# Kernel tuning notes

Measured on AMD Instinct MI355X. Metric: run time of the kernel, lower is better.

Reference implementation:

```python
import jax, jax.numpy as jnp
import numpy as np

N, D_IN, D_OUT, E, K, H = 8192, 256, 256, 16, 2, 512


def setup_inputs() -> dict:
    key = jax.random.key(0)
    ks = jax.random.split(key, 11)
    return {
        "x": jax.random.normal(ks[0], (N, D_IN), jnp.float32),
        "gate_w": jax.random.normal(ks[1], (D_IN, H), jnp.float32),
        "gate_b": jax.random.normal(ks[2], (H,), jnp.float32),
        "gate_out_w": jax.random.normal(ks[3], (H, E), jnp.float32),
        "gate_out_b": jax.random.normal(ks[4], (E,), jnp.float32),
        "mlp_w1": jax.random.normal(ks[5], (D_IN, E, H), jnp.float32),
        "mlp_b1": jax.random.normal(ks[6], (E, H), jnp.float32),
        "mlp_w2": jax.random.normal(ks[7], (H, E, H), jnp.float32),
        "mlp_b2": jax.random.normal(ks[8], (E, H), jnp.float32),
        "mlp_w3": jax.random.normal(ks[9], (H, E, D_OUT), jnp.float32),
        "mlp_b3": jax.random.normal(ks[10], (E, D_OUT), jnp.float32),
    }


def reference(x, gate_w, gate_b, gate_out_w, gate_out_b,
              mlp_w1, mlp_b1, mlp_w2, mlp_b2, mlp_w3, mlp_b3):
    n, e = x.shape[0], gate_out_w.shape[1]
    # Gate MLP: relu(x @ Wg + bg) @ Wo + bo -> [N, E]
    logits = jax.nn.relu(x @ gate_w + gate_b) @ gate_out_w + gate_out_b
    # Top-k expert selection + softmax over selected gate values
    top_vals, top_idx = jax.lax.top_k(logits, K)              # [N, K]
    gates = jax.nn.softmax(top_vals, axis=-1)                 # [N, K]
    # Scatter into a sparse combine matrix [N, E] (top-k indices are unique per row)
    combine = jnp.zeros((n, e), x.dtype).at[jnp.arange(n)[:, None], top_idx].set(gates)
    # Per-expert 3-layer MLP, computed densely over all experts then combined.
    h1 = jax.nn.relu(jnp.einsum('ni,ieh->neh', x, mlp_w1) + mlp_b1)    # [N, E, H]
    h2 = jax.nn.relu(jnp.einsum('neh,heg->neg', h1, mlp_w2) + mlp_b2)  # [N, E, H]
    ye = jnp.einsum('neg,geo->neo', h2, mlp_w3) + mlp_b3               # [N, E, D_OUT]
    # Gate-weighted combine over experts (only top-k contribute)
    return jnp.einsum('neo,ne->no', ye, combine)
```

## Files before the change

kernel.cpp:

```cpp
#include <hip/hip_runtime.h>
#include <hip/hip_bf16.h>
#include <stdint.h>

#define NTOK 8192
#define DIN  256
#define DOUT 256
#define NEXP 16
#define HID  512
#define NKA  (NTOK*2)
#define NBLK (NTOK/256)
#define MAXTILE 272
#define GK 768

typedef __bf16 bf16x8 __attribute__((ext_vector_type(8)));
typedef __bf16 bf16x4 __attribute__((ext_vector_type(4)));
typedef float  f32x4  __attribute__((ext_vector_type(4)));

__device__ __forceinline__ void async_cp16(const __bf16* g, __bf16* l) {
  __builtin_amdgcn_global_load_lds(
      (const __attribute__((address_space(1))) unsigned int*)g,
      (__attribute__((address_space(3))) unsigned int*)l, 16, 0, 0);
}

__global__ void cvt_x_kernel(const float* __restrict__ x, __bf16* __restrict__ xb,
                             __bf16* __restrict__ xs) {
  int i = blockIdx.x * blockDim.x + threadIdx.x;
  float4 v = ((const float4*)x)[i];
  int base = i * 4;
  int t = base >> 8, c = base & 255;
  bf16x4 hi = { (__bf16)v.x, (__bf16)v.y, (__bf16)v.z, (__bf16)v.w };
  bf16x4 lo = { (__bf16)(v.x - (float)hi[0]), (__bf16)(v.y - (float)hi[1]),
                (__bf16)(v.z - (float)hi[2]), (__bf16)(v.w - (float)hi[3]) };
  *(bf16x4*)(xb + (size_t)t * DIN + c) = hi;
  __bf16* row = xs + (size_t)t * GK + c;
  *(bf16x4*)(row)       = hi;
  *(bf16x4*)(row + 256) = lo;
  *(bf16x4*)(row + 512) = hi;
}

__global__ void transpose_cvt_kernel(const float* __restrict__ src, __bf16* __restrict__ dst,
                                     int K, int N) {
  __shared__ float t[32][33];
  int e  = blockIdx.z;
  int k0 = blockIdx.x * 32, n0 = blockIdx.y * 32;
  int tx = threadIdx.x, ty = threadIdx.y;
  #pragma unroll
  for (int j = 0; j < 4; j++) {
    int kl = ty + j * 8;
    t[kl][tx] = src[(size_t)(k0 + kl) * (NEXP * N) + (size_t)e * N + n0 + tx];
  }
  __syncthreads();
  #pragma unroll
  for (int j = 0; j < 4; j++) {
    int nl = ty + j * 8;
    dst[(size_t)e * N * K + (size_t)(n0 + nl) * K + k0 + tx] = (__bf16)t[tx][nl];
  }
}

__global__ void gate_w_split_kernel(const float* __restrict__ gw, __bf16* __restrict__ gwt,
                                    int* __restrict__ gtile_e, int* __restrict__ gtile_mt,
                                    int* __restrict__ gntiles, int* __restrict__ gseg) {
  __shared__ float t[32][33];
  int k0 = blockIdx.x * 32, n0 = blockIdx.y * 32;
  int tx = threadIdx.x, ty = threadIdx.y;
  #pragma unroll
  for (int j = 0; j < 4; j++) {
    int kl = ty + j * 8;
    t[kl][tx] = gw[(size_t)(k0 + kl) * HID + n0 + tx];
  }
  __syncthreads();
  #pragma unroll
  for (int j = 0; j < 4; j++) {
    int nl = ty + j * 8;
    float v = t[tx][nl];
    __bf16 hi = (__bf16)v;
    __bf16 lo = (__bf16)(v - (float)hi);
    __bf16* drow = gwt + (size_t)(n0 + nl) * GK + k0 + tx;
    drow[0]   = hi;
    drow[256] = hi;
    drow[512] = lo;
  }
  if (blockIdx.x == 0 && blockIdx.y == 0) {
    int tid = ty * 32 + tx;
    if (tid < 128) { gtile_e[tid] = 0; gtile_mt[tid] = tid; }
    else if (tid == 128) { *gntiles = 128; }
    else if (tid == 129) { gseg[0] = 0; gseg[1] = NTOK; }
  }
}

__global__ __launch_bounds__(128) void logits_kernel(const float* __restrict__ hg,
                                                     const float* __restrict__ gw,
                                                     const float* __restrict__ gb,
                                                     float* __restrict__ logits) {
  __shared__ float hl[8][HID];
  __shared__ float wl[HID][16];
  int t0 = blockIdx.x * 8;
  int tid = threadIdx.x;
  for (int c = tid; c < 8 * (HID / 4); c += 128) {
    int row = c >> 7, col = (c & 127) * 4;
    *(float4*)&hl[row][col] = *(const float4*)&hg[(size_t)(t0 + row) * HID + col];
  }
  for (int c = tid; c < HID * 4; c += 128) {
    int k = c >> 2, e4 = (c & 3) * 4;
    *(float4*)&wl[k][e4] = *(const float4*)&gw[(size_t)k * 16 + e4];
  }
  __syncthreads();
  int tok = tid >> 4, e = tid & 15;
  float s = gb[e];
  #pragma unroll 8
  for (int k = 0; k < HID; k++) s = fmaf(hl[tok][k], wl[k][e], s);
  logits[(size_t)(t0 + tok) * 16 + e] = s;
}

__global__ __launch_bounds__(256) void top2_route_kernel(const float* __restrict__ logits,
                                                         int2* __restrict__ e01,
                                                         float2* __restrict__ g01,
                                                         int* __restrict__ lrank,
                                                         int* __restrict__ blockhist) {
  __shared__ int hist[NEXP];
  int tid = threadIdx.x;
  if (tid < NEXP) hist[tid] = 0;
  __syncthreads();
  int t = blockIdx.x * 256 + tid;
  float lv[16];
  const float4* lp = (const float4*)(logits + (size_t)t * 16);
  #pragma unroll
  for (int j = 0; j < 4; j++) { float4 v = lp[j]; lv[4*j]=v.x; lv[4*j+1]=v.y; lv[4*j+2]=v.z; lv[4*j+3]=v.w; }
  float v0 = -3.402823466e38f, v1 = -3.402823466e38f;
  int i0 = 0, i1 = 0;
  #pragma unroll
  for (int e = 0; e < 16; e++) {
    float v = lv[e];
    if (v > v0) { v1 = v0; i1 = i0; v0 = v; i0 = e; }
    else if (v > v1) { v1 = v; i1 = e; }
  }
  float ew = expf(v1 - v0);
  float inv = 1.f / (1.f + ew);
  e01[t] = make_int2(i0, i1);
  g01[t] = make_float2(inv, ew * inv);
  int r0 = atomicAdd(&hist[i0], 1);
  int r1 = atomicAdd(&hist[i1], 1);
  lrank[2 * t]     = r0;
  lrank[2 * t + 1] = r1;
  __syncthreads();
  if (tid < NEXP) blockhist[blockIdx.x * NEXP + tid] = hist[tid];
}

__global__ void scan2_kernel(const int* __restrict__ blockhist, int* __restrict__ offsets,
                             int* __restrict__ base, int* __restrict__ tile_e,
                             int* __restrict__ tile_mt, int* __restrict__ ntiles) {
  __shared__ int tot[NEXP];
  __shared__ int soff[NEXP + 1];
  __shared__ int tbase[NEXP];
  int e = threadIdx.x;
  if (e < NEXP) {
    int s = 0;
    for (int b = 0; b < NBLK; b++) s += blockhist[b * NEXP + e];
    tot[e] = s;
  }
  __syncthreads();
  if (e == 0) {
    int s = 0, tb = 0;
    for (int i = 0; i < NEXP; i++) {
      soff[i] = s; s += tot[i];
      tbase[i] = tb; tb += (tot[i] + 63) >> 6;
    }
    soff[NEXP] = s;
    *ntiles = tb;
  }
  __syncthreads();
  if (e < NEXP + 1) offsets[e] = soff[e];
  if (e < NEXP) {
    int s = soff[e];
    for (int b = 0; b < NBLK; b++) { base[b * NEXP + e] = s; s += blockhist[b * NEXP + e]; }
    int nt = (tot[e] + 63) >> 6, tb = tbase[e];
    for (int m = 0; m < nt; m++) { tile_e[tb + m] = e; tile_mt[tb + m] = m; }
  }
}

__global__ __launch_bounds__(256) void fill2_kernel(const int2* __restrict__ e01,
                                                    const int* __restrict__ lrank,
                                                    const int* __restrict__ base,
                                                    int* __restrict__ tok_sorted,
                                                    int* __restrict__ route_pos) {
  int b = blockIdx.x;
  int t = b * 256 + threadIdx.x;
  int2 e = e01[t];
  int p0 = base[b * NEXP + e.x] + lrank[2 * t];
  int p1 = base[b * NEXP + e.y] + lrank[2 * t + 1];
  tok_sorted[p0] = t; route_pos[2 * t]     = p0;
  tok_sorted[p1] = t; route_pos[2 * t + 1] = p1;
}

template<bool OUT_F32, bool RELU>
__global__ __launch_bounds__(256) void moe_gemm_kernel(const __bf16* __restrict__ A,
                                                       const __bf16* __restrict__ Bt,
                                                       const float* __restrict__ bias,
                                                       void* __restrict__ out,
                                                       const int* __restrict__ seg_off,
                                                       const int* __restrict__ gather,
                                                       const int* __restrict__ tile_e,
                                                       const int* __restrict__ tile_mt,
                                                       const int* __restrict__ ntiles,
                                                       int K, int N) {
  int bx = blockIdx.x;
  if (bx >= *ntiles) return;
  int e  = tile_e[bx];
  int mt = tile_mt[bx];
  int off = seg_off[e];
  int Te  = seg_off[e + 1] - off;
  int nt = blockIdx.y;

  __shared__ __bf16 Al[2][64][32];
  __shared__ __bf16 Bl[2][128][32];

  int tid = threadIdx.x;
  int lane = tid & 63, w = tid >> 6;
  int l16 = lane & 15, quad = lane >> 4;

  int r0 = tid >> 2;
  int q8 = ((tid & 3) ^ ((r0 >> 1) & 3)) * 8;
  int rowA = mt * 64 + r0;
  int rA = rowA < Te ? rowA : Te - 1;
  size_t ga = gather ? (size_t)gather[off + rA] : (size_t)(off + rA);
  const __bf16* apg  = A + ga * K + q8;
  const __bf16* Bte  = Bt + (size_t)e * N * K;
  const __bf16* bpg0 = Bte + (size_t)(nt * 128 + r0) * K + q8;
  const __bf16* bpg1 = bpg0 + (size_t)64 * K;

  __bf16* al0 = &Al[0][0][0];
  __bf16* al1 = &Al[1][0][0];
  __bf16* bl0 = &Bl[0][0][0];
  __bf16* bl1 = &Bl[1][0][0];

  f32x4 acc[4][2];
  #pragma unroll
  for (int i = 0; i < 4; i++)
    #pragma unroll
    for (int j = 0; j < 2; j++) acc[i][j] = {0.f, 0.f, 0.f, 0.f};

  async_cp16(apg, al0 + tid * 8);
  async_cp16(bpg0, bl0 + tid * 8);
  async_cp16(bpg1, bl0 + (tid + 256) * 8);

  int qs = (quad ^ ((l16 >> 1) & 3)) * 8;

  int nIter = K >> 5;
  for (int it = 0; it < nIter; ++it) {
    int buf = it & 1;
    if (it + 1 < nIter) {
      int kb = (it + 1) << 5;
      __bf16* an = buf ? al0 : al1;
      __bf16* bn = buf ? bl0 : bl1;
      async_cp16(apg + kb, an + tid * 8);
      async_cp16(bpg0 + kb, bn + tid * 8);
      async_cp16(bpg1 + kb, bn + (tid + 256) * 8);
      asm volatile("s_waitcnt vmcnt(3)" ::: "memory");
    } else {
      asm volatile("s_waitcnt vmcnt(0)" ::: "memory");
    }
    __builtin_amdgcn_s_barrier();
    asm volatile("" ::: "memory");
    const __bf16* ab = buf ? al1 : al0;
    const __bf16* bb = buf ? bl1 : bl0;
    bf16x8 af[4], bfr[2];
    #pragma unroll
    for (int i = 0; i < 4; i++)
      af[i] = *(const bf16x8*)(ab + (size_t)(i * 16 + l16) * 32 + qs);
    #pragma unroll
    for (int i = 0; i < 2; i++)
      bfr[i] = *(const bf16x8*)(bb + (size_t)(w * 32 + i * 16 + l16) * 32 + qs);
    #pragma unroll
    for (int mi = 0; mi < 4; mi++)
      #pragma unroll
      for (int ni = 0; ni < 2; ni++)
        acc[mi][ni] = __builtin_amdgcn_mfma_f32_16x16x32_bf16(af[mi], bfr[ni], acc[mi][ni], 0, 0, 0);
    asm volatile("" ::: "memory");
    __builtin_amdgcn_s_barrier();
  }

  const float* be = bias + (size_t)e * N;
  #pragma unroll
  for (int ni = 0; ni < 2; ni++) {
    int col = nt * 128 + w * 32 + ni * 16 + l16;
    float bv = be[col];
    #pragma unroll
    for (int mi = 0; mi < 4; mi++) {
      #pragma unroll
      for (int r = 0; r < 4; r++) {
        int row_in = mt * 64 + mi * 16 + quad * 4 + r;
        if (row_in < Te) {
          float v = acc[mi][ni][r] + bv;
          if (RELU) v = fmaxf(v, 0.f);
          size_t orow = (size_t)(off + row_in);
          if (OUT_F32) ((float*)out)[orow * N + col] = v;
          else ((__bf16*)out)[orow * N + col] = (__bf16)v;
        }
      }
    }
  }
}

__global__ void combine_kernel(const float* __restrict__ Y, const int* __restrict__ route_pos,
                               const float2* __restrict__ g01, float* __restrict__ out) {
  int gid = blockIdx.x * blockDim.x + threadIdx.x;
  int t = gid >> 6, c = (gid & 63) << 2;
  if (t >= NTOK) return;
  int p0 = route_pos[2 * t], p1 = route_pos[2 * t + 1];
  float2 g = g01[t];
  float4 y0 = *(const float4*)&Y[(size_t)p0 * DOUT + c];
  float4 y1 = *(const float4*)&Y[(size_t)p1 * DOUT + c];
  float4 o;
  o.x = g.x * y0.x + g.y * y1.x;
  o.y = g.x * y0.y + g.y * y1.y;
  o.z = g.x * y0.z + g.y * y1.z;
  o.w = g.x * y0.w + g.y * y1.w;
  *(float4*)&out[(size_t)t * DOUT + c] = o;
}

extern "C" void kernel_launch(void* const* d_in, const int* in_sizes, int n_in,
                              void* d_out, int out_size, void* d_ws, size_t ws_size,
                              hipStream_t stream) {
  const float* x          = (const float*)d_in[0];
  const float* gate_w     = (const float*)d_in[1];
  const float* gate_b     = (const float*)d_in[2];
  const float* gate_out_w = (const float*)d_in[3];
  const float* gate_out_b = (const float*)d_in[4];
  const float* w1         = (const float*)d_in[5];
  const float* b1         = (const float*)d_in[6];
  const float* w2         = (const float*)d_in[7];
  const float* b2         = (const float*)d_in[8];
  const float* w3         = (const float*)d_in[9];
  const float* b3         = (const float*)d_in[10];
  float* out = (float*)d_out;

  char* ws = (char*)d_ws;
  size_t o = 0;
  auto alloc = [&](size_t bytes) -> void* {
    o = (o + 255) & ~(size_t)255;
    void* p = ws + o;
    o += bytes;
    return p;
  };

  __bf16* xb   = (__bf16*)alloc((size_t)NTOK * DIN * 2);
  __bf16* w1t  = (__bf16*)alloc((size_t)NEXP * HID * DIN * 2);
  __bf16* w2t  = (__bf16*)alloc((size_t)NEXP * HID * HID * 2);
  __bf16* w3t  = (__bf16*)alloc((size_t)NEXP * DOUT * HID * 2);
  __bf16* gwt  = (__bf16*)alloc((size_t)HID * GK * 2);
  size_t r1 = (size_t)NTOK * HID * 4;
  size_t r2 = (size_t)(NKA + 128) * HID * 2;
  void* region1 = alloc(r1 > r2 ? r1 : r2);
  float*  hg = (float*)region1;
  __bf16* H1 = (__bf16*)region1;
  size_t r3 = (size_t)NTOK * GK * 2;
  size_t r4 = (size_t)(NKA + 128) * HID * 2;
  void* region2 = alloc(r3 > r4 ? r3 : r4);
  __bf16* xs = (__bf16*)region2;
  __bf16* H2 = (__bf16*)region2;
  float* logits    = (float*)alloc((size_t)NTOK * 16 * 4);
  int2*  e01       = (int2*)alloc((size_t)NTOK * 8);
  float2* g01      = (float2*)alloc((size_t)NTOK * 8);
  int*   offsets   = (int*)alloc((NEXP + 1) * 4);
  int*   blockhist = (int*)alloc((size_t)NBLK * NEXP * 4);
  int*   base      = (int*)alloc((size_t)NBLK * NEXP * 4);
  int*   lrank     = (int*)alloc((size_t)NTOK * 2 * 4);
  int*   tok_sorted= (int*)alloc((size_t)(NKA + 128) * 4);
  int*   route_pos = (int*)alloc((size_t)NTOK * 2 * 4);
  int*   tile_e    = (int*)alloc(MAXTILE * 4);
  int*   tile_mt   = (int*)alloc(MAXTILE * 4);
  int*   ntiles    = (int*)alloc(4);
  int*   gtile_e   = (int*)alloc(128 * 4);
  int*   gtile_mt  = (int*)alloc(128 * 4);
  int*   gntiles   = (int*)alloc(4);
  int*   gseg      = (int*)alloc(2 * 4);
  float*  Y        = (float*)alloc((size_t)(NKA + 128) * DOUT * 4);
  (void)ws_size; (void)n_in; (void)in_sizes; (void)out_size;

  cvt_x_kernel<<<(NTOK * DIN / 4) / 256, 256, 0, stream>>>(x, xb, xs);

  dim3 tb(32, 8);
  gate_w_split_kernel<<<dim3(DIN / 32, HID / 32), tb, 0, stream>>>(
      gate_w, gwt, gtile_e, gtile_mt, gntiles, gseg);
  transpose_cvt_kernel<<<dim3(DIN / 32, HID / 32, NEXP), tb, 0, stream>>>(w1, w1t, DIN, HID);
  transpose_cvt_kernel<<<dim3(HID / 32, HID / 32, NEXP), tb, 0, stream>>>(w2, w2t, HID, HID);
  transpose_cvt_kernel<<<dim3(HID / 32, DOUT / 32, NEXP), tb, 0, stream>>>(w3, w3t, HID, DOUT);

  moe_gemm_kernel<true, true><<<dim3(NTOK / 64, HID / 128), 256, 0, stream>>>(
      xs, gwt, gate_b, hg, gseg, nullptr, gtile_e, gtile_mt, gntiles, GK, HID);

  logits_kernel<<<NTOK / 8, 128, 0, stream>>>(hg, gate_out_w, gate_out_b, logits);
  top2_route_kernel<<<NBLK, 256, 0, stream>>>(logits, e01, g01, lrank, blockhist);
  scan2_kernel<<<1, 64, 0, stream>>>(blockhist, offsets, base, tile_e, tile_mt, ntiles);
  fill2_kernel<<<NBLK, 256, 0, stream>>>(e01, lrank, base, tok_sorted, route_pos);

  moe_gemm_kernel<false, true><<<dim3(MAXTILE, HID / 128), 256, 0, stream>>>(
      xb, w1t, b1, H1, offsets, tok_sorted, tile_e, tile_mt, ntiles, DIN, HID);
  moe_gemm_kernel<false, true><<<dim3(MAXTILE, HID / 128), 256, 0, stream>>>(
      H1, w2t, b2, H2, offsets, nullptr, tile_e, tile_mt, ntiles, HID, HID);
  moe_gemm_kernel<true, false><<<dim3(MAXTILE, DOUT / 128), 256, 0, stream>>>(
      H2, w3t, b3, Y, offsets, nullptr, tile_e, tile_mt, ntiles, HID, DOUT);

  combine_kernel<<<(NTOK * 64) / 256, 256, 0, stream>>>(Y, route_pos, g01, out);
}
```

Measured before the change: 233.1 us.

## Fuse prep conversions into one launch and merge logits with top-2 routing

All input and weight conversion kernels (x split, gate weight split, three expert weight transposes) are merged into a single prep_kernel dispatched by block index. This cuts four launches and their gaps. The logits and top-2 routing kernels are fused into a route_kernel that keeps logits in shared memory, removing the logits buffer round trip. Histograms are now per 8-token block (1024 blocks), so the scan kernel is parallelised over 256 threads with a two-level prefix, and fill2 indexes base by t>>3.

After: 223.8 us. -4.0%, faster.

```diff
diff --git a/kernel.cpp b/kernel.cpp
--- a/kernel.cpp
+++ b/kernel.cpp
@@ -9,6 +9,7 @@
 #define HID  512
 #define NKA  (NTOK*2)
 #define NBLK (NTOK/256)
+#define NRBLK (NTOK/8)
 #define MAXTILE 272
 #define GK 768
 
@@ -22,28 +23,11 @@
       (__attribute__((address_space(3))) unsigned int*)l, 16, 0, 0);
 }
 
-__global__ void cvt_x_kernel(const float* __restrict__ x, __bf16* __restrict__ xb,
-                             __bf16* __restrict__ xs) {
-  int i = blockIdx.x * blockDim.x + threadIdx.x;
-  float4 v = ((const float4*)x)[i];
-  int base = i * 4;
-  int t = base >> 8, c = base & 255;
-  bf16x4 hi = { (__bf16)v.x, (__bf16)v.y, (__bf16)v.z, (__bf16)v.w };
-  bf16x4 lo = { (__bf16)(v.x - (float)hi[0]), (__bf16)(v.y - (float)hi[1]),
-                (__bf16)(v.z - (float)hi[2]), (__bf16)(v.w - (float)hi[3]) };
-  *(bf16x4*)(xb + (size_t)t * DIN + c) = hi;
-  __bf16* row = xs + (size_t)t * GK + c;
-  *(bf16x4*)(row)       = hi;
-  *(bf16x4*)(row + 256) = lo;
-  *(bf16x4*)(row + 512) = hi;
-}
-
-__global__ void transpose_cvt_kernel(const float* __restrict__ src, __bf16* __restrict__ dst,
-                                     int K, int N) {
-  __shared__ float t[32][33];
-  int e  = blockIdx.z;
-  int k0 = blockIdx.x * 32, n0 = blockIdx.y * 32;
-  int tx = threadIdx.x, ty = threadIdx.y;
+__device__ __forceinline__ void transpose_cvt_body(const float* __restrict__ src,
+                                                   __bf16* __restrict__ dst,
+                                                   int K, int N, int bx, int by, int bz,
+                                                   int tx, int ty, float (*t)[33]) {
+  int e = bz, k0 = bx * 32, n0 = by * 32;
   #pragma unroll
   for (int j = 0; j < 4; j++) {
     int kl = ty + j * 8;
@@ -57,45 +41,82 @@
   }
 }
 
-__global__ void gate_w_split_kernel(const float* __restrict__ gw, __bf16* __restrict__ gwt,
-                                    int* __restrict__ gtile_e, int* __restrict__ gtile_mt,
-                                    int* __restrict__ gntiles, int* __restrict__ gseg) {
+__global__ __launch_bounds__(256) void prep_kernel(
+    const float* __restrict__ x, __bf16* __restrict__ xb, __bf16* __restrict__ xs,
+    const float* __restrict__ gw, __bf16* __restrict__ gwt,
+    const float* __restrict__ w1, __bf16* __restrict__ w1t,
+    const float* __restrict__ w2, __bf16* __restrict__ w2t,
+    const float* __restrict__ w3, __bf16* __restrict__ w3t,
+    int* __restrict__ gtile_e, int* __restrict__ gtile_mt,
+    int* __restrict__ gntiles, int* __restrict__ gseg) {
   __shared__ float t[32][33];
-  int k0 = blockIdx.x * 32, n0 = blockIdx.y * 32;
-  int tx = threadIdx.x, ty = threadIdx.y;
-  #pragma unroll
-  for (int j = 0; j < 4; j++) {
-    int kl = ty + j * 8;
-    t[kl][tx] = gw[(size_t)(k0 + kl) * HID + n0 + tx];
-  }
-  __syncthreads();
-  #pragma unroll
-  for (int j = 0; j < 4; j++) {
-    int nl = ty + j * 8;
-    float v = t[tx][nl];
-    __bf16 hi = (__bf16)v;
-    __bf16 lo = (__bf16)(v - (float)hi);
-    __bf16* drow = gwt + (size_t)(n0 + nl) * GK + k0 + tx;
-    drow[0]   = hi;
-    drow[256] = hi;
-    drow[512] = lo;
-  }
-  if (blockIdx.x == 0 && blockIdx.y == 0) {
-    int tid = ty * 32 + tx;
-    if (tid < 128) { gtile_e[tid] = 0; gtile_mt[tid] = tid; }
-    else if (tid == 128) { *gntiles = 128; }
-    else if (tid == 129) { gseg[0] = 0; gseg[1] = NTOK; }
-  }
-}
-
-__global__ __launch_bounds__(128) void logits_kernel(const float* __restrict__ hg,
-                                                     const float* __restrict__ gw,
-                                                     const float* __restrict__ gb,
-                                                     float* __restrict__ logits) {
-  __shared__ float hl[8][HID];
+  int idx = blockIdx.x;
+  int tid = threadIdx.x;
+  int tx = tid & 31, ty = tid >> 5;
+  if (idx < 2048) {
+    int i = idx * 256 + tid;
+    float4 v = ((const float4*)x)[i];
+    int base = i * 4;
+    int tk = base >> 8, c = base & 255;
+    bf16x4 hi = { (__bf16)v.x, (__bf16)v.y, (__bf16)v.z, (__bf16)v.w };
+    bf16x4 lo = { (__bf16)(v.x - (float)hi[0]), (__bf16)(v.y - (float)hi[1]),
+                  (__bf16)(v.z - (float)hi[2]), (__bf16)(v.w - (float)hi[3]) };
+    *(bf16x4*)(xb + (size_t)tk * DIN + c) = hi;
+    __bf16* row = xs + (size_t)tk * GK + c;
+    *(bf16x4*)(row)       = hi;
+    *(bf16x4*)(row + 256) = lo;
+    *(bf16x4*)(row + 512) = hi;
+  } else if (idx < 2176) {
+    int g = idx - 2048;
+    int k0 = (g & 7) * 32, n0 = (g >> 3) * 32;
+    #pragma unroll
+    for (int j = 0; j < 4; j++) {
+      int kl = ty + j * 8;
+      t[kl][tx] = gw[(size_t)(k0 + kl) * HID + n0 + tx];
+    }
+    __syncthreads();
+    #pragma unroll
+    for (int j = 0; j < 4; j++) {
+      int nl = ty + j * 8;
+      float v = t[tx][nl];
+      __bf16 hi = (__bf16)v;
+      __bf16 lo = (__bf16)(v - (float)hi);
+      __bf16* drow = gwt + (size_t)(n0 + nl) * GK + k0 + tx;
+      drow[0]   = hi;
+      drow[256] = hi;
+      drow[512] = lo;
+    }
+    if (g == 0) {
+      if (tid < 128) { gtile_e[tid] = 0; gtile_mt[tid] = tid; }
+      else if (tid == 128) { *gntiles = 128; }
+      else if (tid == 129) { gseg[0] = 0; gseg[1] = NTOK; }
+    }
+  } else if (idx < 4224) {
+    int g = idx - 2176;
+    transpose_cvt_body(w1, w1t, DIN, HID, g & 7, (g >> 3) & 15, g >> 7, tx, ty, t);
+  } else if (idx < 8320) {
+    int g = idx - 4224;
+    transpose_cvt_body(w2, w2t, HID, HID, g & 15, (g >> 4) & 15, g >> 8, tx, ty, t);
+  } else {
+    int g = idx - 8320;
+    transpose_cvt_body(w3, w3t, HID, DOUT, g & 15, (g >> 4) & 7, g >> 7, tx, ty, t);
+  }
+}
+
+__global__ __launch_bounds__(128) void route_kernel(const float* __restrict__ hg,
+                                                    const float* __restrict__ gw,
+                                                    const float* __restrict__ gb,
+                                                    int2* __restrict__ e01,
+                                                    float2* __restrict__ g01,
+                                                    int* __restrict__ lrank,
+                                                    int* __restrict__ blockhist) {
+  __shared__ float hl[8][HID + 8];
   __shared__ float wl[HID][16];
+  __shared__ float ls[8][16];
+  __shared__ int bhist[NEXP];
   int t0 = blockIdx.x * 8;
   int tid = threadIdx.x;
+  if (tid < NEXP) bhist[tid] = 0;
   for (int c = tid; c < 8 * (HID / 4); c += 128) {
     int row = c >> 7, col = (c & 127) * 4;
     *(float4*)&hl[row][col] = *(const float4*)&hg[(size_t)(t0 + row) * HID + col];
@@ -109,72 +130,76 @@
   float s = gb[e];
   #pragma unroll 8
   for (int k = 0; k < HID; k++) s = fmaf(hl[tok][k], wl[k][e], s);
-  logits[(size_t)(t0 + tok) * 16 + e] = s;
-}
-
-__global__ __launch_bounds__(256) void top2_route_kernel(const float* __restrict__ logits,
-                                                         int2* __restrict__ e01,
-                                                         float2* __restrict__ g01,
-                                                         int* __restrict__ lrank,
-                                                         int* __restrict__ blockhist) {
-  __shared__ int hist[NEXP];
-  int tid = threadIdx.x;
-  if (tid < NEXP) hist[tid] = 0;
-  __syncthreads();
-  int t = blockIdx.x * 256 + tid;
-  float lv[16];
-  const float4* lp = (const float4*)(logits + (size_t)t * 16);
-  #pragma unroll
-  for (int j = 0; j < 4; j++) { float4 v = lp[j]; lv[4*j]=v.x; lv[4*j+1]=v.y; lv[4*j+2]=v.z; lv[4*j+3]=v.w; }
-  float v0 = -3.402823466e38f, v1 = -3.402823466e38f;
-  int i0 = 0, i1 = 0;
-  #pragma unroll
-  for (int e = 0; e < 16; e++) {
-    float v = lv[e];
-    if (v > v0) { v1 = v0; i1 = i0; v0 = v; i0 = e; }
-    else if (v > v1) { v1 = v; i1 = e; }
-  }
-  float ew = expf(v1 - v0);
-  float inv = 1.f / (1.f + ew);
-  e01[t] = make_int2(i0, i1);
-  g01[t] = make_float2(inv, ew * inv);
-  int r0 = atomicAdd(&hist[i0], 1);
-  int r1 = atomicAdd(&hist[i1], 1);
-  lrank[2 * t]     = r0;
-  lrank[2 * t + 1] = r1;
-  __syncthreads();
-  if (tid < NEXP) blockhist[blockIdx.x * NEXP + tid] = hist[tid];
-}
-
-__global__ void scan2_kernel(const int* __restrict__ blockhist, int* __restrict__ offsets,
-                             int* __restrict__ base, int* __restrict__ tile_e,
-                             int* __restrict__ tile_mt, int* __restrict__ ntiles) {
+  ls[tok][e] = s;
+  __syncthreads();
+  if (tid < 8) {
+    int t = t0 + tid;
+    float v0 = -3.402823466e38f, v1 = -3.402823466e38f;
+    int i0 = 0, i1 = 0;
+    #pragma unroll
+    for (int ee = 0; ee < 16; ee++) {
+      float v = ls[tid][ee];
+      if (v > v0) { v1 = v0; i1 = i0; v0 = v; i0 = ee; }
+      else if (v > v1) { v1 = v; i1 = ee; }
+    }
+    float ew = expf(v1 - v0);
+    float inv = 1.f / (1.f + ew);
+    e01[t] = make_int2(i0, i1);
+    g01[t] = make_float2(inv, ew * inv);
+    int r0 = atomicAdd(&bhist[i0], 1);
+    int r1 = atomicAdd(&bhist[i1], 1);
+    lrank[2 * t]     = r0;
+    lrank[2 * t + 1] = r1;
+  }
+  __syncthreads();
+  if (tid < NEXP) blockhist[blockIdx.x * NEXP + tid] = bhist[tid];
+}
+
+__global__ __launch_bounds__(256) void scan2_kernel(const int* __restrict__ blockhist,
+                                                    int* __restrict__ offsets,
+                                                    int* __restrict__ base,
+                                                    int* __restrict__ tile_e,
+                                                    int* __restrict__ tile_mt,
+                                                    int* __restrict__ ntiles) {
+  __shared__ int part[NEXP][16];
+  __shared__ int cbase[NEXP][16];
   __shared__ int tot[NEXP];
   __shared__ int soff[NEXP + 1];
   __shared__ int tbase[NEXP];
-  int e = threadIdx.x;
-  if (e < NEXP) {
-    int s = 0;
-    for (int b = 0; b < NBLK; b++) s += blockhist[b * NEXP + e];
-    tot[e] = s;
-  }
-  __syncthreads();
-  if (e == 0) {
-    int s = 0, tb = 0;
+  int tid = threadIdx.x;
+  int e = tid & 15, c = tid >> 4;
+  int s = 0;
+  for (int i = 0; i < 64; i++) s += blockhist[(size_t)(c * 64 + i) * NEXP + e];
+  part[e][c] = s;
+  __syncthreads();
+  if (tid < NEXP) {
+    int t = 0;
+    for (int c2 = 0; c2 < 16; c2++) { cbase[tid][c2] = t; t += part[tid][c2]; }
+    tot[tid] = t;
+  }
+  __syncthreads();
+  if (tid == 0) {
+    int acc = 0, tb = 0;
     for (int i = 0; i < NEXP; i++) {
-      soff[i] = s; s += tot[i];
+      soff[i] = acc; acc += tot[i];
       tbase[i] = tb; tb += (tot[i] + 63) >> 6;
     }
-    soff[NEXP] = s;
+    soff[NEXP] = acc;
     *ntiles = tb;
   }
   __syncthreads();
-  if (e < NEXP + 1) offsets[e] = soff[e];
-  if (e < NEXP) {
-    int s = soff[e];
-    for (int b = 0; b < NBLK; b++) { base[b * NEXP + e] = s; s += blockhist[b * NEXP + e]; }
-    int nt = (tot[e] + 63) >> 6, tb = tbase[e];
-    for (int m = 0; m < nt; m++) { tile_e[tb + m] = e; tile_mt[tb + m] = m; }
+  if (tid < NEXP + 1) offsets[tid] = soff[tid];
+  {
+    int run = soff[e] + cbase[e][c];
+    for (int i = 0; i < 64; i++) {
+      int b = c * 64 + i;
+      base[(size_t)b * NEXP + e] = run;
+      run += blockhist[(size_t)b * NEXP + e];
+    }
+  }
+  if (tid < NEXP) {
+    int nt = (tot[tid] + 63) >> 6, tb = tbase[tid];
+    for (int m = 0; m < nt; m++) { tile_e[tb + m] = tid; tile_mt[tb + m] = m; }
   }
 }
 
@@ -183,11 +208,11 @@
                                                     const int* __restrict__ base,
                                                     int* __restrict__ tok_sorted,
                                                     int* __restrict__ route_pos) {
-  int b = blockIdx.x;
-  int t = b * 256 + threadIdx.x;
+  int t = blockIdx.x * 256 + threadIdx.x;
   int2 e = e01[t];
-  int p0 = base[b * NEXP + e.x] + lrank[2 * t];
-  int p1 = base[b * NEXP + e.y] + lrank[2 * t + 1];
+  int b = t >> 3;
+  int p0 = base[(size_t)b * NEXP + e.x] + lrank[2 * t];
+  int p1 = base[(size_t)b * NEXP + e.y] + lrank[2 * t + 1];
   tok_sorted[p0] = t; route_pos[2 * t]     = p0;
   tok_sorted[p1] = t; route_pos[2 * t + 1] = p1;
 }
@@ -358,12 +383,11 @@
   void* region2 = alloc(r3 > r4 ? r3 : r4);
   __bf16* xs = (__bf16*)region2;
   __bf16* H2 = (__bf16*)region2;
-  float* logits    = (float*)alloc((size_t)NTOK * 16 * 4);
   int2*  e01       = (int2*)alloc((size_t)NTOK * 8);
   float2* g01      = (float2*)alloc((size_t)NTOK * 8);
   int*   offsets   = (int*)alloc((NEXP + 1) * 4);
-  int*   blockhist = (int*)alloc((size_t)NBLK * NEXP * 4);
-  int*   base      = (int*)alloc((size_t)NBLK * NEXP * 4);
+  int*   blockhist = (int*)alloc((size_t)NRBLK * NEXP * 4);
+  int*   base      = (int*)alloc((size_t)NRBLK * NEXP * 4);
   int*   lrank     = (int*)alloc((size_t)NTOK * 2 * 4);
   int*   tok_sorted= (int*)alloc((size_t)(NKA + 128) * 4);
   int*   route_pos = (int*)alloc((size_t)NTOK * 2 * 4);
@@ -377,21 +401,16 @@
   float*  Y        = (float*)alloc((size_t)(NKA + 128) * DOUT * 4);
   (void)ws_size; (void)n_in; (void)in_sizes; (void)out_size;
 
-  cvt_x_kernel<<<(NTOK * DIN / 4) / 256, 256, 0, stream>>>(x, xb, xs);
-
-  dim3 tb(32, 8);
-  gate_w_split_kernel<<<dim3(DIN / 32, HID / 32), tb, 0, stream>>>(
-      gate_w, gwt, gtile_e, gtile_mt, gntiles, gseg);
-  transpose_cvt_kernel<<<dim3(DIN / 32, HID / 32, NEXP), tb, 0, stream>>>(w1, w1t, DIN, HID);
-  transpose_cvt_kernel<<<dim3(HID / 32, HID / 32, NEXP), tb, 0, stream>>>(w2, w2t, HID, HID);
-  transpose_cvt_kernel<<<dim3(HID / 32, DOUT / 32, NEXP), tb, 0, stream>>>(w3, w3t, HID, DOUT);
+  prep_kernel<<<10368, 256, 0, stream>>>(x, xb, xs, gate_w, gwt,
+                                         w1, w1t, w2, w2t, w3, w3t,
+                                         gtile_e, gtile_mt, gntiles, gseg);
 
   moe_gemm_kernel<true, true><<<dim3(NTOK / 64, HID / 128), 256, 0, stream>>>(
       xs, gwt, gate_b, hg, gseg, nullptr, gtile_e, gtile_mt, gntiles, GK, HID);
 
-  logits_kernel<<<NTOK / 8, 128, 0, stream>>>(hg, gate_out_w, gate_out_b, logits);
-  top2_route_kernel<<<NBLK, 256, 0, stream>>>(logits, e01, g01, lrank, blockhist);
-  scan2_kernel<<<1, 64, 0, stream>>>(blockhist, offsets, base, tile_e, tile_mt, ntiles);
+  route_kernel<<<NTOK / 8, 128, 0, stream>>>(hg, gate_out_w, gate_out_b,
+                                             e01, g01, lrank, blockhist);
+  scan2_kernel<<<1, 256, 0, stream>>>(blockhist, offsets, base, tile_e, tile_mt, ntiles);
   fill2_kernel<<<NBLK, 256, 0, stream>>>(e01, lrank, base, tok_sorted, route_pos);
 
   moe_gemm_kernel<false, true><<<dim3(MAXTILE, HID / 128), 256, 0, stream>>>(
```

## Merge prep kernels into one launch and fuse gate logits into gate GEMM epilogue

Applied to the files above, without the earlier changes.

Folds the x conversion, gate-weight split, three expert-weight transposes and a logits zero-fill into a single prep kernel keyed on block index. This cuts several launches and their tail gaps. The gate GEMM now does the second gate layer in its epilogue: the ReLU hidden tile goes to LDS, is multiplied by a slice of gate_out_w, and partial logits are atomically added. That removes the fp32 hidden-state write/read and the separate logits kernel, with the output bias moved into top2. The cost is float atomics, which make logit sums order-nondeterministic and could in rare cases flip top-2 ties.

Result: faster. 202.5 us (-13.1%).

```diff
diff --git a/kernel.cpp b/kernel.cpp
--- a/kernel.cpp
+++ b/kernel.cpp
@@ -22,28 +22,11 @@
       (__attribute__((address_space(3))) unsigned int*)l, 16, 0, 0);
 }
 
-__global__ void cvt_x_kernel(const float* __restrict__ x, __bf16* __restrict__ xb,
-                             __bf16* __restrict__ xs) {
-  int i = blockIdx.x * blockDim.x + threadIdx.x;
-  float4 v = ((const float4*)x)[i];
-  int base = i * 4;
-  int t = base >> 8, c = base & 255;
-  bf16x4 hi = { (__bf16)v.x, (__bf16)v.y, (__bf16)v.z, (__bf16)v.w };
-  bf16x4 lo = { (__bf16)(v.x - (float)hi[0]), (__bf16)(v.y - (float)hi[1]),
-                (__bf16)(v.z - (float)hi[2]), (__bf16)(v.w - (float)hi[3]) };
-  *(bf16x4*)(xb + (size_t)t * DIN + c) = hi;
-  __bf16* row = xs + (size_t)t * GK + c;
-  *(bf16x4*)(row)       = hi;
-  *(bf16x4*)(row + 256) = lo;
-  *(bf16x4*)(row + 512) = hi;
-}
-
-__global__ void transpose_cvt_kernel(const float* __restrict__ src, __bf16* __restrict__ dst,
-                                     int K, int N) {
-  __shared__ float t[32][33];
-  int e  = blockIdx.z;
-  int k0 = blockIdx.x * 32, n0 = blockIdx.y * 32;
-  int tx = threadIdx.x, ty = threadIdx.y;
+__device__ __forceinline__ void transpose_cvt_body(const float* __restrict__ src,
+                                                   __bf16* __restrict__ dst,
+                                                   int K, int N, int bx, int by, int bz,
+                                                   int tx, int ty, float (*t)[33]) {
+  int e = bz, k0 = bx * 32, n0 = by * 32;
   #pragma unroll
   for (int j = 0; j < 4; j++) {
     int kl = ty + j * 8;
@@ -57,75 +40,94 @@
   }
 }
 
-__global__ void gate_w_split_kernel(const float* __restrict__ gw, __bf16* __restrict__ gwt,
-                                    int* __restrict__ gtile_e, int* __restrict__ gtile_mt,
-                                    int* __restrict__ gntiles, int* __restrict__ gseg) {
+__global__ __launch_bounds__(256) void prep_kernel(
+    const float* __restrict__ x, __bf16* __restrict__ xb, __bf16* __restrict__ xs,
+    const float* __restrict__ gw, __bf16* __restrict__ gwt,
+    const float* __restrict__ w1, __bf16* __restrict__ w1t,
+    const float* __restrict__ w2, __bf16* __restrict__ w2t,
+    const float* __restrict__ w3, __bf16* __restrict__ w3t,
+    int* __restrict__ gtile_e, int* __restrict__ gtile_mt,
+    int* __restrict__ gntiles, int* __restrict__ gseg,
+    float* __restrict__ logitz) {
   __shared__ float t[32][33];
-  int k0 = blockIdx.x * 32, n0 = blockIdx.y * 32;
-  int tx = threadIdx.x, ty = threadIdx.y;
-  #pragma unroll
-  for (int j = 0; j < 4; j++) {
-    int kl = ty + j * 8;
-    t[kl][tx] = gw[(size_t)(k0 + kl) * HID + n0 + tx];
-  }
-  __syncthreads();
-  #pragma unroll
-  for (int j = 0; j < 4; j++) {
-    int nl = ty + j * 8;
-    float v = t[tx][nl];
-    __bf16 hi = (__bf16)v;
-    __bf16 lo = (__bf16)(v - (float)hi);
-    __bf16* drow = gwt + (size_t)(n0 + nl) * GK + k0 + tx;
-    drow[0]   = hi;
-    drow[256] = hi;
-    drow[512] = lo;
-  }
-  if (blockIdx.x == 0 && blockIdx.y == 0) {
-    int tid = ty * 32 + tx;
-    if (tid < 128) { gtile_e[tid] = 0; gtile_mt[tid] = tid; }
-    else if (tid == 128) { *gntiles = 128; }
-    else if (tid == 129) { gseg[0] = 0; gseg[1] = NTOK; }
-  }
-}
-
-__global__ __launch_bounds__(128) void logits_kernel(const float* __restrict__ hg,
-                                                     const float* __restrict__ gw,
-                                                     const float* __restrict__ gb,
-                                                     float* __restrict__ logits) {
-  __shared__ float hl[8][HID];
-  __shared__ float wl[HID][16];
-  int t0 = blockIdx.x * 8;
+  int idx = blockIdx.x;
   int tid = threadIdx.x;
-  for (int c = tid; c < 8 * (HID / 4); c += 128) {
-    int row = c >> 7, col = (c & 127) * 4;
-    *(float4*)&hl[row][col] = *(const float4*)&hg[(size_t)(t0 + row) * HID + col];
-  }
-  for (int c = tid; c < HID * 4; c += 128) {
-    int k = c >> 2, e4 = (c & 3) * 4;
-    *(float4*)&wl[k][e4] = *(const float4*)&gw[(size_t)k * 16 + e4];
-  }
-  __syncthreads();
-  int tok = tid >> 4, e = tid & 15;
-  float s = gb[e];
-  #pragma unroll 8
-  for (int k = 0; k < HID; k++) s = fmaf(hl[tok][k], wl[k][e], s);
-  logits[(size_t)(t0 + tok) * 16 + e] = s;
-}
-
-__global__ __launch_bounds__(256) void top2_route_kernel(const float* __restrict__ logits,
-                                                         int2* __restrict__ e01,
-                                                         float2* __restrict__ g01,
-                                                         int* __restrict__ lrank,
-                                                         int* __restrict__ blockhist) {
+  int tx = tid & 31, ty = tid >> 5;
+  if (idx < 2048) {
+    int i = idx * 256 + tid;
+    float4 v = ((const float4*)x)[i];
+    int base = i * 4;
+    int tk = base >> 8, c = base & 255;
+    bf16x4 hi = { (__bf16)v.x, (__bf16)v.y, (__bf16)v.z, (__bf16)v.w };
+    bf16x4 lo = { (__bf16)(v.x - (float)hi[0]), (__bf16)(v.y - (float)hi[1]),
+                  (__bf16)(v.z - (float)hi[2]), (__bf16)(v.w - (float)hi[3]) };
+    *(bf16x4*)(xb + (size_t)tk * DIN + c) = hi;
+    __bf16* row = xs + (size_t)tk * GK + c;
+    *(bf16x4*)(row)       = hi;
+    *(bf16x4*)(row + 256) = lo;
+    *(bf16x4*)(row + 512) = hi;
+  } else if (idx < 2176) {
+    int g = idx - 2048;
+    int k0 = (g & 7) * 32, n0 = (g >> 3) * 32;
+    #pragma unroll
+    for (int j = 0; j < 4; j++) {
+      int kl = ty + j * 8;
+      t[kl][tx] = gw[(size_t)(k0 + kl) * HID + n0 + tx];
+    }
+    __syncthreads();
+    #pragma unroll
+    for (int j = 0; j < 4; j++) {
+      int nl = ty + j * 8;
+      float v = t[tx][nl];
+      __bf16 hi = (__bf16)v;
+      __bf16 lo = (__bf16)(v - (float)hi);
+      __bf16* drow = gwt + (size_t)(n0 + nl) * GK + k0 + tx;
+      drow[0]   = hi;
+      drow[256] = hi;
+      drow[512] = lo;
+    }
+    if (g == 0) {
+      if (tid < 128) { gtile_e[tid] = 0; gtile_mt[tid] = tid; }
+      else if (tid == 128) { *gntiles = 128; }
+      else if (tid == 129) { gseg[0] = 0; gseg[1] = NTOK; }
+    }
+  } else if (idx < 4224) {
+    int g = idx - 2176;
+    transpose_cvt_body(w1, w1t, DIN, HID, g & 7, (g >> 3) & 15, g >> 7, tx, ty, t);
+  } else if (idx < 8320) {
+    int g = idx - 4224;
+    transpose_cvt_body(w2, w2t, HID, HID, g & 15, (g >> 4) & 15, g >> 8, tx, ty, t);
+  } else if (idx < 10368) {
+    int g = idx - 8320;
+    transpose_cvt_body(w3, w3t, HID, DOUT, g & 15, (g >> 4) & 7, g >> 7, tx, ty, t);
+  } else {
+    int i = (idx - 10368) * 256 + tid;
+    ((float4*)logitz)[i] = make_float4(0.f, 0.f, 0.f, 0.f);
+  }
+}
+
+__global__ __launch_bounds__(256) void top2_kernel(const float* __restrict__ logits,
+                                                   const float* __restrict__ gb,
+                                                   int2* __restrict__ e01,
+                                                   float2* __restrict__ g01,
+                                                   int* __restrict__ lrank,
+                                                   int* __restrict__ blockhist) {
   __shared__ int hist[NEXP];
+  __shared__ float gbl[NEXP];
   int tid = threadIdx.x;
-  if (tid < NEXP) hist[tid] = 0;
+  if (tid < NEXP) { hist[tid] = 0; gbl[tid] = gb[tid]; }
   __syncthreads();
   int t = blockIdx.x * 256 + tid;
   float lv[16];
   const float4* lp = (const float4*)(logits + (size_t)t * 16);
   #pragma unroll
-  for (int j = 0; j < 4; j++) { float4 v = lp[j]; lv[4*j]=v.x; lv[4*j+1]=v.y; lv[4*j+2]=v.z; lv[4*j+3]=v.w; }
+  for (int j = 0; j < 4; j++) {
+    float4 v = lp[j];
+    lv[4*j]   = v.x + gbl[4*j];
+    lv[4*j+1] = v.y + gbl[4*j+1];
+    lv[4*j+2] = v.z + gbl[4*j+2];
+    lv[4*j+3] = v.w + gbl[4*j+3];
+  }
   float v0 = -3.402823466e38f, v1 = -3.402823466e38f;
   int i0 = 0, i1 = 0;
   #pragma unroll
@@ -192,7 +194,7 @@
   tok_sorted[p1] = t; route_pos[2 * t + 1] = p1;
 }
 
-template<bool OUT_F32, bool RELU>
+template<int MODE, bool RELU>
 __global__ __launch_bounds__(256) void moe_gemm_kernel(const __bf16* __restrict__ A,
                                                        const __bf16* __restrict__ Bt,
                                                        const float* __restrict__ bias,
@@ -202,6 +204,7 @@
                                                        const int* __restrict__ tile_e,
                                                        const int* __restrict__ tile_mt,
                                                        const int* __restrict__ ntiles,
+                                                       const float* __restrict__ gow,
                                                        int K, int N) {
   int bx = blockIdx.x;
   if (bx >= *ntiles) return;
@@ -211,8 +214,10 @@
   int Te  = seg_off[e + 1] - off;
   int nt = blockIdx.y;
 
-  __shared__ __bf16 Al[2][64][32];
-  __shared__ __bf16 Bl[2][128][32];
+  constexpr int SMEM = (MODE == 3) ? (8192 + 64 * 132 * 4) : 24576;
+  __shared__ __align__(16) char smem[SMEM];
+  __bf16* AlB = (__bf16*)smem;
+  __bf16* BlB = (__bf16*)(smem + 8192);
 
   int tid = threadIdx.x;
   int lane = tid & 63, w = tid >> 6;
@@ -228,10 +233,10 @@
   const __bf16* bpg0 = Bte + (size_t)(nt * 128 + r0) * K + q8;
   const __bf16* bpg1 = bpg0 + (size_t)64 * K;
 
-  __bf16* al0 = &Al[0][0][0];
-  __bf16* al1 = &Al[1][0][0];
-  __bf16* bl0 = &Bl[0][0][0];
-  __bf16* bl1 = &Bl[1][0][0];
+  __bf16* al0 = AlB;
+  __bf16* al1 = AlB + 2048;
+  __bf16* bl0 = BlB;
+  __bf16* bl1 = BlB + 4096;
 
   f32x4 acc[4][2];
   #pragma unroll
@@ -280,6 +285,49 @@
   }
 
   const float* be = bias + (size_t)e * N;
+  if (MODE == 3) {
+    __syncthreads();
+    float* wl = (float*)smem;
+    float* ht = (float*)(smem + 8192);
+    if (tid < 128) {
+      const float* gr = gow + (size_t)(nt * 128 + tid) * 16;
+      #pragma unroll
+      for (int j = 0; j < 4; j++)
+        *(float4*)&wl[tid * 16 + j * 4] = *(const float4*)&gr[j * 4];
+    }
+    float bv[2];
+    #pragma unroll
+    for (int ni = 0; ni < 2; ni++) bv[ni] = be[nt * 128 + w * 32 + ni * 16 + l16];
+    #pragma unroll
+    for (int mi = 0; mi < 4; mi++)
+      #pragma unroll
+      for (int ni = 0; ni < 2; ni++)
+        #pragma unroll
+        for (int r = 0; r < 4; r++) {
+          int row = mi * 16 + quad * 4 + r;
+          int col = w * 32 + ni * 16 + l16;
+          ht[row * 132 + col] = fmaxf(acc[mi][ni][r] + bv[ni], 0.f);
+        }
+    __syncthreads();
+    int t = tid >> 2, e4 = (tid & 3) * 4;
+    float s0 = 0.f, s1 = 0.f, s2 = 0.f, s3 = 0.f;
+    #pragma unroll 4
+    for (int h = 0; h < 128; h++) {
+      float hv = ht[t * 132 + h];
+      const float* wr = &wl[h * 16 + e4];
+      s0 = fmaf(hv, wr[0], s0);
+      s1 = fmaf(hv, wr[1], s1);
+      s2 = fmaf(hv, wr[2], s2);
+      s3 = fmaf(hv, wr[3], s3);
+    }
+    float* lp = (float*)out + (size_t)(mt * 64 + t) * 16 + e4;
+    atomicAdd(lp + 0, s0);
+    atomicAdd(lp + 1, s1);
+    atomicAdd(lp + 2, s2);
+    atomicAdd(lp + 3, s3);
+    return;
+  }
+
   #pragma unroll
   for (int ni = 0; ni < 2; ni++) {
     int col = nt * 128 + w * 32 + ni * 16 + l16;
@@ -293,7 +341,7 @@
           float v = acc[mi][ni][r] + bv;
           if (RELU) v = fmaxf(v, 0.f);
           size_t orow = (size_t)(off + row_in);
-          if (OUT_F32) ((float*)out)[orow * N + col] = v;
+          if (MODE == 1) ((float*)out)[orow * N + col] = v;
           else ((__bf16*)out)[orow * N + col] = (__bf16)v;
         }
       }
@@ -348,11 +396,7 @@
   __bf16* w2t  = (__bf16*)alloc((size_t)NEXP * HID * HID * 2);
   __bf16* w3t  = (__bf16*)alloc((size_t)NEXP * DOUT * HID * 2);
   __bf16* gwt  = (__bf16*)alloc((size_t)HID * GK * 2);
-  size_t r1 = (size_t)NTOK * HID * 4;
-  size_t r2 = (size_t)(NKA + 128) * HID * 2;
-  void* region1 = alloc(r1 > r2 ? r1 : r2);
-  float*  hg = (float*)region1;
-  __bf16* H1 = (__bf16*)region1;
+  __bf16* H1   = (__bf16*)alloc((size_t)(NKA + 128) * HID * 2);
   size_t r3 = (size_t)NTOK * GK * 2;
   size_t r4 = (size_t)(NKA + 128) * HID * 2;
   void* region2 = alloc(r3 > r4 ? r3 : r4);
@@ -377,29 +421,27 @@
   float*  Y        = (float*)alloc((size_t)(NKA + 128) * DOUT * 4);
   (void)ws_size; (void)n_in; (void)in_sizes; (void)out_size;
 
-  cvt_x_kernel<<<(NTOK * DIN / 4) / 256, 256, 0, stream>>>(x, xb, xs);
-
-  dim3 tb(32, 8);
-  gate_w_split_kernel<<<dim3(DIN / 32, HID / 32), tb, 0, stream>>>(
-      gate_w, gwt, gtile_e, gtile_mt, gntiles, gseg);
-  transpose_cvt_kernel<<<dim3(DIN / 32, HID / 32, NEXP), tb, 0, stream>>>(w1, w1t, DIN, HID);
-  transpose_cvt_kernel<<<dim3(HID / 32, HID / 32, NEXP), tb, 0, stream>>>(w2, w2t, HID, HID);
-  transpose_cvt_kernel<<<dim3(HID / 32, DOUT / 32, NEXP), tb, 0, stream>>>(w3, w3t, HID, DOUT);
-
-  moe_gemm_kernel<true, true><<<dim3(NTOK / 64, HID / 128), 256, 0, stream>>>(
-      xs, gwt, gate_b, hg, gseg, nullptr, gtile_e, gtile_mt, gntiles, GK, HID);
-
-  logits_kernel<<<NTOK / 8, 128, 0, stream>>>(hg, gate_out_w, gate_out_b, logits);
-  top2_route_kernel<<<NBLK, 256, 0, stream>>>(logits, e01, g01, lrank, blockhist);
+  prep_kernel<<<10496, 256, 0, stream>>>(x, xb, xs, gate_w, gwt,
+                                         w1, w1t, w2, w2t, w3, w3t,
+                                         gtile_e, gtile_mt, gntiles, gseg, logits);
+
+  moe_gemm_kernel<3, true><<<dim3(NTOK / 64, HID / 128), 256, 0, stream>>>(
+      xs, gwt, gate_b, logits, gseg, nullptr, gtile_e, gtile_mt, gntiles,
+      gate_out_w, GK, HID);
+
+  top2_kernel<<<NBLK, 256, 0, stream>>>(logits, gate_out_b, e01, g01, lrank, blockhist);
   scan2_kernel<<<1, 64, 0, stream>>>(blockhist, offsets, base, tile_e, tile_mt, ntiles);
   fill2_kernel<<<NBLK, 256, 0, stream>>>(e01, lrank, base, tok_sorted, route_pos);
 
-  moe_gemm_kernel<false, true><<<dim3(MAXTILE, HID / 128), 256, 0, stream>>>(
-      xb, w1t, b1, H1, offsets, tok_sorted, tile_e, tile_mt, ntiles, DIN, HID);
-  moe_gemm_kernel<false, true><<<dim3(MAXTILE, HID / 128), 256, 0, stream>>>(
-      H1, w2t, b2, H2, offsets, nullptr, tile_e, tile_mt, ntiles, HID, HID);
-  moe_gemm_kernel<true, false><<<dim3(MAXTILE, DOUT / 128), 256, 0, stream>>>(
-      H2, w3t, b3, Y, offsets, nullptr, tile_e, tile_mt, ntiles, HID, DOUT);
+  moe_gemm_kernel<0, true><<<dim3(MAXTILE, HID / 128), 256, 0, stream>>>(
+      xb, w1t, b1, H1, offsets, tok_sorted, tile_e, tile_mt, ntiles,
+      nullptr, DIN, HID);
+  moe_gemm_kernel<0, true><<<dim3(MAXTILE, HID / 128), 256, 0, stream>>>(
+      H1, w2t, b2, H2, offsets, nullptr, tile_e, tile_mt, ntiles,
+      nullptr, HID, HID);
+  moe_gemm_kernel<1, false><<<dim3(MAXTILE, DOUT / 128), 256, 0, stream>>>(
+      H2, w3t, b3, Y, offsets, nullptr, tile_e, tile_mt, ntiles,
+      nullptr, HID, DOUT);
 
   combine_kernel<<<(NTOK * 64) / 256, 256, 0, stream>>>(Y, route_pos, g01, out);
 }
```
